# Kernel tuning notes

Measured on AMD Instinct MI355X. Metric: run time of the kernel, lower is better.

## Reference

```python
import jax, jax.numpy as jnp
import numpy as np

INTRA_W, TYPE_W, INTER_W = 1.0, 0.5, 0.5
MARGIN, TAU, EPS = 1.0, 0.1, 1e-8
N, D = 200000, 256          # nodes, feature dim
NT, EPT = 4, 2048           # n types, edges per type
E = NT * EPT                # 8192 hyperedges
SAMP_PER_TYPE = 100         # max_edges_per_type for intra loss
MAX_PAIRS = 500             # inter-loss pair sample


def setup_inputs() -> dict:
    key = jax.random.key(0)
    k1, k2, k3, k4, k5 = jax.random.split(key, 5)
    z_nodes = jax.random.normal(k1, (N, D), dtype=jnp.float32)
    # deterministic variable edge sizes in [8, 56]
    sizes = 8 + (np.arange(E) * 7919) % 49
    M = int(sizes.sum())  # 262128
    member_edge_id = jnp.asarray(np.repeat(np.arange(E), sizes), dtype=jnp.int32)
    member_node_idx = jax.random.randint(k2, (M,), 0, N, dtype=jnp.int32)
    edge_type = jnp.asarray(np.repeat(np.arange(NT), EPT), dtype=jnp.int32)
    # intra-loss edge sampling: 100 edges per type (mimics torch.randperm sampling)
    perm = jax.random.permutation(k3, EPT)
    intra_sample = jnp.concatenate(
        [perm[:SAMP_PER_TYPE] + t * EPT for t in range(NT)]).astype(jnp.int32)
    # inter-loss pair sampling (mimics torch.randint + self-collision fixup)
    pair_idx1 = jax.random.randint(k4, (MAX_PAIRS,), 0, E, dtype=jnp.int32)
    pair_idx2 = jax.random.randint(k5, (MAX_PAIRS,), 0, E, dtype=jnp.int32)
    pair_idx2 = jnp.where(pair_idx1 == pair_idx2, (pair_idx2 + 1) % E, pair_idx2)
    return dict(z_nodes=z_nodes, member_node_idx=member_node_idx,
                member_edge_id=member_edge_id, edge_type=edge_type,
                intra_sample=intra_sample, pair_idx1=pair_idx1, pair_idx2=pair_idx2)


def reference(z_nodes, member_node_idx, member_edge_id, edge_type,
              intra_sample, pair_idx1, pair_idx2):
    # --- ragged segment mean: hyperedge embeddings ---
    gathered = z_nodes[member_node_idx]                               # [M, D]
    counts = jax.ops.segment_sum(jnp.ones_like(member_edge_id, jnp.float32),
                                 member_edge_id, num_segments=E)      # [E]
    edge_sum = jax.ops.segment_sum(gathered, member_edge_id, num_segments=E)
    edge_emb = edge_sum / counts[:, None]                             # [E, D]

    # --- B1: intra-hyperedge loss over sampled edges ---
    sq_dist = jnp.sum((gathered - edge_emb[member_edge_id]) ** 2, axis=-1)  # [M]
    per_edge = jax.ops.segment_sum(sq_dist, member_edge_id, num_segments=E) / counts
    intra = jnp.mean(per_edge[intra_sample])

    # --- B2: type contrastive InfoNCE ---
    z = edge_emb / jnp.linalg.norm(edge_emb, axis=-1, keepdims=True)  # [E, D]
    sim = jnp.matmul(z, z.T) / TAU                                    # [E, E]
    self_mask = jnp.eye(E, dtype=bool)
    exp_sim = jnp.exp(sim) * (~self_mask)
    denom = exp_sim.sum(axis=1)
    type_mask = (edge_type[None, :] == edge_type[:, None]) & ~self_mask
    numer = jnp.sum(exp_sim * type_mask, axis=1)
    per_row = -jnp.log((numer + EPS) / (denom + EPS))
    has_pos = type_mask.sum(axis=1) > 0
    type_loss = jnp.sum(jnp.where(has_pos, per_row, 0.0)) / jnp.maximum(
        has_pos.sum().astype(per_row.dtype), 1.0)

    # --- B3: inter-hyperedge margin loss on sampled pairs ---
    dist = jnp.linalg.norm(edge_emb[pair_idx1] - edge_emb[pair_idx2], axis=-1)
    inter = jnp.mean(jax.nn.relu(MARGIN - dist) ** 2)

    total = INTRA_W * intra + TYPE_W * type_loss + INTER_W * inter
    return jnp.stack([intra, type_loss, inter, total])
```

## Files before the change

kernel.cpp:

```cpp
#include <hip/hip_runtime.h>


#define DDIM 256
#define NTYPES 4
#define TAU_INV 10.0f
#define EPSV 1e-8f

#define COLSEG 512
#define CTILE 32
#define NTILES (COLSEG / CTILE)
#define BPAD 264

typedef short v8s __attribute__((ext_vector_type(8)));
typedef float v4f __attribute__((ext_vector_type(4)));
typedef unsigned short ushort_t;

__device__ __forceinline__ int lower_bound_i(const int* __restrict__ a, int n, int key) {
  int lo = 0, hi = n;
  while (lo < hi) { int mid = (lo + hi) >> 1; if (a[mid] < key) lo = mid + 1; else hi = mid; }
  return lo;
}

__device__ __forceinline__ ushort_t f2bf(float f) {
  union { float f; unsigned u; } v; v.f = f;
  unsigned r = v.u + 0x7FFFu + ((v.u >> 16) & 1u);
  return (ushort_t)(r >> 16);
}

__device__ __forceinline__ float bf2f(ushort_t u) {
  union { unsigned u; float f; } v; v.u = ((unsigned)u) << 16;
  return v.f;
}

__global__ __launch_bounds__(256)
void edge_kernel(const float* __restrict__ z, const int* __restrict__ mni,
                 const int* __restrict__ mei, int M, int E,
                 ushort_t* __restrict__ zn, float* __restrict__ emb,
                 float* __restrict__ per_edge, float* __restrict__ typeSums,
                 float* __restrict__ selfArr, float* __restrict__ scalars) {
  __shared__ int shIdx[64];
  __shared__ float shAcc[1024];
  __shared__ float shRed[12];
  int e = blockIdx.x;
  int tid = threadIdx.x;
  if (tid < NTYPES) typeSums[e * NTYPES + tid] = 0.f;
  if (e == 0 && tid >= 16 && tid < 24) scalars[tid - 16] = 0.f;

  int s = lower_bound_i(mei, M, e);
  int t = lower_bound_i(mei, M, e + 1);
  int cnt = t - s;
  if (tid < cnt) shIdx[tid] = mni[s + tid];
  __syncthreads();

  int group = tid >> 6, lane = tid & 63;
  float4 acc = make_float4(0.f, 0.f, 0.f, 0.f);
  float sq = 0.f;
  int m = group;
  for (; m + 12 < cnt; m += 16) {
    int n0 = shIdx[m], n1 = shIdx[m + 4], n2 = shIdx[m + 8], n3 = shIdx[m + 12];
    float4 v0 = *(const float4*)(z + (size_t)n0 * DDIM + lane * 4);
    float4 v1 = *(const float4*)(z + (size_t)n1 * DDIM + lane * 4);
    float4 v2 = *(const float4*)(z + (size_t)n2 * DDIM + lane * 4);
    float4 v3 = *(const float4*)(z + (size_t)n3 * DDIM + lane * 4);
    acc.x += v0.x; acc.y += v0.y; acc.z += v0.z; acc.w += v0.w;
    sq += v0.x * v0.x + v0.y * v0.y + v0.z * v0.z + v0.w * v0.w;
    acc.x += v1.x; acc.y += v1.y; acc.z += v1.z; acc.w += v1.w;
    sq += v1.x * v1.x + v1.y * v1.y + v1.z * v1.z + v1.w * v1.w;
    acc.x += v2.x; acc.y += v2.y; acc.z += v2.z; acc.w += v2.w;
    sq += v2.x * v2.x + v2.y * v2.y + v2.z * v2.z + v2.w * v2.w;
    acc.x += v3.x; acc.y += v3.y; acc.z += v3.z; acc.w += v3.w;
    sq += v3.x * v3.x + v3.y * v3.y + v3.z * v3.z + v3.w * v3.w;
  }
  for (; m < cnt; m += 4) {
    int n0 = shIdx[m];
    float4 v0 = *(const float4*)(z + (size_t)n0 * DDIM + lane * 4);
    acc.x += v0.x; acc.y += v0.y; acc.z += v0.z; acc.w += v0.w;
    sq += v0.x * v0.x + v0.y * v0.y + v0.z * v0.z + v0.w * v0.w;
  }

  *(float4*)(&shAcc[tid * 4]) = acc;
  __syncthreads();
  int d = tid;
  float total = shAcc[d] + shAcc[256 + d] + shAcc[512 + d] + shAcc[768 + d];
  float inv = 1.0f / (float)cnt;
  float mu = total * inv;
  emb[(size_t)e * DDIM + d] = mu;

  float a1 = sq, a2 = mu * mu;
  #pragma unroll
  for (int off = 32; off > 0; off >>= 1) {
    a1 += __shfl_down(a1, off);
    a2 += __shfl_down(a2, off);
  }
  if (lane == 0) { shRed[group] = a1; shRed[4 + group] = a2; }
  __syncthreads();
  if (tid == 0) {
    float sqT = shRed[0] + shRed[1] + shRed[2] + shRed[3];
    float musqT = shRed[4] + shRed[5] + shRed[6] + shRed[7];
    per_edge[e] = sqT * inv - musqT;
    shRed[8] = musqT;
  }
  __syncthreads();
  float rn = rsqrtf(shRed[8]);
  ushort_t znv = f2bf(mu * rn);
  zn[(size_t)e * DDIM + d] = znv;

  float zq = bf2f(znv);
  float a3 = zq * zq;
  #pragma unroll
  for (int off = 32; off > 0; off >>= 1) a3 += __shfl_down(a3, off);
  if (lane == 0) shRed[group] = a3;
  __syncthreads();
  if (tid == 0)
    selfArr[e] = __expf(TAU_INV * (shRed[0] + shRed[1] + shRed[2] + shRed[3]));
}

__global__ __launch_bounds__(256)
void gemm_kernel(const ushort_t* __restrict__ zn, const int* __restrict__ edge_type,
                 int E, float* __restrict__ typeSums) {
  __shared__ __align__(16) ushort_t sB[2][CTILE * BPAD];

  int tid = threadIdx.x;
  int lane = tid & 63, wave = tid >> 6;
  int quad = lane >> 4, l15 = lane & 15;
  int rb = blockIdx.y;
  int cs = blockIdx.x;
  int row0 = rb * 256 + wave * 64;
  int c0 = cs * COLSEG;
  int T = edge_type[c0];

  v8s aF[4][8];
  #pragma unroll
  for (int rt = 0; rt < 4; ++rt) {
    const ushort_t* base = zn + (size_t)(row0 + rt * 16 + l15) * DDIM + quad * 8;
    #pragma unroll
    for (int ks = 0; ks < 8; ++ks)
      aF[rt][ks] = *(const v8s*)(base + ks * 32);
  }

  float acc[4][4] = {};

  v8s r[4];
  #pragma unroll
  for (int i = 0; i < 4; ++i) {
    int id = i * 256 + tid, col = id >> 5, c8 = id & 31;
    r[i] = *(const v8s*)(zn + (size_t)(c0 + col) * DDIM + c8 * 8);
  }
  #pragma unroll
  for (int i = 0; i < 4; ++i) {
    int id = i * 256 + tid, col = id >> 5, c8 = id & 31;
    *(v8s*)(&sB[0][col * BPAD + c8 * 8]) = r[i];
  }
  __syncthreads();

  for (int t = 0; t < NTILES; ++t) {
    v8s rn_[4];
    if (t < NTILES - 1) {
      int colb = c0 + (t + 1) * CTILE;
      #pragma unroll
      for (int i = 0; i < 4; ++i) {
        int id = i * 256 + tid, col = id >> 5, c8 = id & 31;
        rn_[i] = *(const v8s*)(zn + (size_t)(colb + col) * DDIM + c8 * 8);
      }
    }

    v4f c[4][2];
    #pragma unroll
    for (int rt = 0; rt < 4; ++rt)
      #pragma unroll
      for (int ct = 0; ct < 2; ++ct)
        c[rt][ct] = (v4f){0.f, 0.f, 0.f, 0.f};

    const ushort_t* buf = sB[t & 1];
    #pragma unroll
    for (int ks = 0; ks < 8; ++ks) {
      #pragma unroll
      for (int ct = 0; ct < 2; ++ct) {
        v8s b = *(const v8s*)(&buf[(ct * 16 + l15) * BPAD + ks * 32 + quad * 8]);
        #pragma unroll
        for (int rt = 0; rt < 4; ++rt)
          c[rt][ct] = __builtin_amdgcn_mfma_f32_16x16x32_bf16(aF[rt][ks], b, c[rt][ct], 0, 0, 0);
      }
    }

    #pragma unroll
    for (int rt = 0; rt < 4; ++rt)
      #pragma unroll
      for (int ct = 0; ct < 2; ++ct)
        #pragma unroll
        for (int rr = 0; rr < 4; ++rr)
          acc[rt][rr] += __expf(c[rt][ct][rr] * TAU_INV);

    if (t < NTILES - 1) {
      int nb = (t + 1) & 1;
      #pragma unroll
      for (int i = 0; i < 4; ++i) {
        int id = i * 256 + tid, col = id >> 5, c8 = id & 31;
        *(v8s*)(&sB[nb][col * BPAD + c8 * 8]) = rn_[i];
      }
    }
    __syncthreads();
  }

  #pragma unroll
  for (int rt = 0; rt < 4; ++rt) {
    #pragma unroll
    for (int rr = 0; rr < 4; ++rr) {
      float v = acc[rt][rr];
      v += __shfl_xor(v, 1);
      v += __shfl_xor(v, 2);
      v += __shfl_xor(v, 4);
      v += __shfl_xor(v, 8);
      if (l15 == 0) {
        int row = row0 + rt * 16 + quad * 4 + rr;
        atomicAdd(&typeSums[row * NTYPES + T], v);
      }
    }
  }
}

__global__ __launch_bounds__(256)
void tail_kernel(const float* __restrict__ emb, const float* __restrict__ per_edge,
                 const int* __restrict__ intra_sample, int nIntra,
                 const int* __restrict__ p1, const int* __restrict__ p2, int nPairs,
                 const float* __restrict__ typeSums, const float* __restrict__ selfArr,
                 const int* __restrict__ edge_type, int E, float* __restrict__ scalars) {
  __shared__ float sh[8];
  int b = blockIdx.x;
  int tid = threadIdx.x;
  int lane = tid & 63, wave = tid >> 6;
  int nRowBlocks = E / 256;

  if (b < nRowBlocks) {
    int row = b * 256 + tid;
    int t = edge_type[row];
    float self = selfArr[row];
    float s0 = typeSums[row * 4 + 0];
    float s1 = typeSums[row * 4 + 1];
    float s2 = typeSums[row * 4 + 2];
    float s3 = typeSums[row * 4 + 3];
    float denom = (s0 + s1 + s2 + s3) - self;
    float own = (t == 0) ? s0 : (t == 1) ? s1 : (t == 2) ? s2 : s3;
    float numer = own - self;
    float pr = 0.f, hp = 0.f;
    int cs = lower_bound_i(edge_type, E, t);
    int ce = lower_bound_i(edge_type, E, t + 1);
    if (ce - cs - 1 > 0) {
      hp = 1.f;
      pr = -__logf((numer + EPSV) / (denom + EPSV));
    }
    float a1 = pr, a2 = hp;
    #pragma unroll
    for (int off = 32; off > 0; off >>= 1) {
      a1 += __shfl_down(a1, off);
      a2 += __shfl_down(a2, off);
    }
    if (lane == 0) { sh[wave] = a1; sh[4 + wave] = a2; }
    __syncthreads();
    if (tid == 0) {
      atomicAdd(&scalars[2], sh[0] + sh[1] + sh[2] + sh[3]);
      atomicAdd(&scalars[3], sh[4] + sh[5] + sh[6] + sh[7]);
    }
  } else if (b == nRowBlocks) {
    float s = 0.f;
    for (int i = tid; i < nIntra; i += 256) s += per_edge[intra_sample[i]];
    #pragma unroll
    for (int off = 32; off > 0; off >>= 1) s += __shfl_down(s, off);
    if (lane == 0) sh[wave] = s;
    __syncthreads();
    if (tid == 0) atomicAdd(&scalars[0], sh[0] + sh[1] + sh[2] + sh[3]);
  } else {
    int p = (b - nRowBlocks - 1) * 4 + wave;
    if (p < nPairs) {
      int i1 = p1[p], i2 = p2[p];
      const float4* r1 = (const float4*)(emb + (size_t)i1 * DDIM);
      const float4* r2 = (const float4*)(emb + (size_t)i2 * DDIM);
      float4 x = r1[lane], y = r2[lane];
      float d0 = x.x - y.x, d1 = x.y - y.y, d2 = x.z - y.z, d3 = x.w - y.w;
      float s = d0 * d0 + d1 * d1 + d2 * d2 + d3 * d3;
      #pragma unroll
      for (int off = 32; off > 0; off >>= 1) s += __shfl_down(s, off);
      if (lane == 0) {
        float dist = sqrtf(s);
        float v = fmaxf(1.0f - dist, 0.0f);
        atomicAdd(&scalars[1], v * v);
      }
    }
  }
}

__global__ void finalize_kernel(const float* __restrict__ scalars, int nIntra, int nPairs,
                                float* __restrict__ out) {
  if (threadIdx.x == 0) {
    float intra = scalars[0] / (float)nIntra;
    float inter = scalars[1] / (float)nPairs;
    float typeL = scalars[2] / fmaxf(scalars[3], 1.f);
    out[0] = intra;
    out[1] = typeL;
    out[2] = inter;
    out[3] = 1.0f * intra + 0.5f * typeL + 0.5f * inter;
  }
}

extern "C" void kernel_launch(void* const* d_in, const int* in_sizes, int n_in,
                              void* d_out, int out_size, void* d_ws, size_t ws_size,
                              hipStream_t stream) {
  const float* z      = (const float*)d_in[0];
  const int* mni      = (const int*)d_in[1];
  const int* mei      = (const int*)d_in[2];
  const int* etype    = (const int*)d_in[3];
  const int* intra_s  = (const int*)d_in[4];
  const int* p1       = (const int*)d_in[5];
  const int* p2       = (const int*)d_in[6];
  int M      = in_sizes[1];
  int E      = in_sizes[3];
  int nIntra = in_sizes[4];
  int nPairs = in_sizes[5];

  char* ws = (char*)d_ws;
  ushort_t* zn    = (ushort_t*)ws;
  float* emb      = (float*)(ws + (size_t)E * DDIM * 2);
  float* per_edge = (float*)(ws + (size_t)E * DDIM * 6);
  float* typeSums = per_edge + E;
  float* selfArr  = typeSums + (size_t)E * NTYPES;
  float* scalars  = selfArr + E;

  float* out = (float*)d_out;

  edge_kernel<<<E, 256, 0, stream>>>(z, mni, mei, M, E, zn, emb, per_edge,
                                     typeSums, selfArr, scalars);

  dim3 g(E / COLSEG, E / 256);
  gemm_kernel<<<g, 256, 0, stream>>>(zn, etype, E, typeSums);

  int nPB = (nPairs + 3) / 4;
  tail_kernel<<<E / 256 + 1 + nPB, 256, 0, stream>>>(
      emb, per_edge, intra_s, nIntra, p1, p2, nPairs,
      typeSums, selfArr, etype, E, scalars);

  finalize_kernel<<<1, 64, 0, stream>>>(scalars, nIntra, nPairs, out);
}
```

Baseline: 354.7 us.

## Precompute segment offsets and load GEMM B fragments directly from global

Adds a boundary kernel that computes each edge's member offsets once, replacing the per-block binary searches in the edge kernel; it also takes over zeroing typeSums and scalars. The GEMM kernel drops the shared-memory double-buffered B tile and instead has each wave load its B fragments straight from global into registers, with ping-pong prefetch across 16-column tiles. Launch bounds now request two blocks per SM. The aim is to remove LDS traffic, barriers and the search latency, at the cost of redundant global/L2 reads of B across waves and higher register pressure.

Result: slower. 372.0 us (+4.9%).

```diff
diff --git a/kernel.cpp b/kernel.cpp
--- a/kernel.cpp
+++ b/kernel.cpp
@@ -7,9 +7,7 @@
 #define EPSV 1e-8f
 
 #define COLSEG 512
-#define CTILE 32
-#define NTILES (COLSEG / CTILE)
-#define BPAD 264
+#define NCT (COLSEG / 16)
 
 typedef short v8s __attribute__((ext_vector_type(8)));
 typedef float v4f __attribute__((ext_vector_type(4)));
@@ -33,21 +31,32 @@
 }
 
 __global__ __launch_bounds__(256)
+void boundary_kernel(const int* __restrict__ mei, int M, int E,
+                     int* __restrict__ off, float* __restrict__ typeSums,
+                     float* __restrict__ scalars) {
+  int i = blockIdx.x * 256 + threadIdx.x;
+  if (i < M - 1) {
+    int a = mei[i], b = mei[i + 1];
+    for (int e = a + 1; e <= b; ++e) off[e] = i + 1;
+  }
+  if (i == 0) { off[0] = 0; off[E] = M; }
+  if (i < E * NTYPES) typeSums[i] = 0.f;
+  if (i < 8) scalars[i] = 0.f;
+}
+
+__global__ __launch_bounds__(256)
 void edge_kernel(const float* __restrict__ z, const int* __restrict__ mni,
-                 const int* __restrict__ mei, int M, int E,
+                 const int* __restrict__ off, int M, int E,
                  ushort_t* __restrict__ zn, float* __restrict__ emb,
-                 float* __restrict__ per_edge, float* __restrict__ typeSums,
-                 float* __restrict__ selfArr, float* __restrict__ scalars) {
+                 float* __restrict__ per_edge, float* __restrict__ selfArr) {
   __shared__ int shIdx[64];
   __shared__ float shAcc[1024];
   __shared__ float shRed[12];
   int e = blockIdx.x;
   int tid = threadIdx.x;
-  if (tid < NTYPES) typeSums[e * NTYPES + tid] = 0.f;
-  if (e == 0 && tid >= 16 && tid < 24) scalars[tid - 16] = 0.f;
-
-  int s = lower_bound_i(mei, M, e);
-  int t = lower_bound_i(mei, M, e + 1);
+
+  int s = off[e];
+  int t = off[e + 1];
   int cnt = t - s;
   if (tid < cnt) shIdx[tid] = mni[s + tid];
   __syncthreads();
@@ -88,9 +97,9 @@
 
   float a1 = sq, a2 = mu * mu;
   #pragma unroll
-  for (int off = 32; off > 0; off >>= 1) {
-    a1 += __shfl_down(a1, off);
-    a2 += __shfl_down(a2, off);
+  for (int off2 = 32; off2 > 0; off2 >>= 1) {
+    a1 += __shfl_down(a1, off2);
+    a2 += __shfl_down(a2, off2);
   }
   if (lane == 0) { shRed[group] = a1; shRed[4 + group] = a2; }
   __syncthreads();
@@ -108,18 +117,16 @@
   float zq = bf2f(znv);
   float a3 = zq * zq;
   #pragma unroll
-  for (int off = 32; off > 0; off >>= 1) a3 += __shfl_down(a3, off);
+  for (int off2 = 32; off2 > 0; off2 >>= 1) a3 += __shfl_down(a3, off2);
   if (lane == 0) shRed[group] = a3;
   __syncthreads();
   if (tid == 0)
     selfArr[e] = __expf(TAU_INV * (shRed[0] + shRed[1] + shRed[2] + shRed[3]));
 }
 
-__global__ __launch_bounds__(256)
+__global__ __launch_bounds__(256, 2)
 void gemm_kernel(const ushort_t* __restrict__ zn, const int* __restrict__ edge_type,
                  int E, float* __restrict__ typeSums) {
-  __shared__ __align__(16) ushort_t sB[2][CTILE * BPAD];
-
   int tid = threadIdx.x;
   int lane = tid & 63, wave = tid >> 6;
   int quad = lane >> 4, l15 = lane & 15;
@@ -140,66 +147,36 @@
 
   float acc[4][4] = {};
 
-  v8s r[4];
-  #pragma unroll
-  for (int i = 0; i < 4; ++i) {
-    int id = i * 256 + tid, col = id >> 5, c8 = id & 31;
-    r[i] = *(const v8s*)(zn + (size_t)(c0 + col) * DDIM + c8 * 8);
-  }
-  #pragma unroll
-  for (int i = 0; i < 4; ++i) {
-    int id = i * 256 + tid, col = id >> 5, c8 = id & 31;
-    *(v8s*)(&sB[0][col * BPAD + c8 * 8]) = r[i];
-  }
-  __syncthreads();
-
-  for (int t = 0; t < NTILES; ++t) {
-    v8s rn_[4];
-    if (t < NTILES - 1) {
-      int colb = c0 + (t + 1) * CTILE;
+  const ushort_t* bbase = zn + (size_t)(c0 + l15) * DDIM + quad * 8;
+
+  v8s b0[8], b1[8];
+  #pragma unroll
+  for (int ks = 0; ks < 8; ++ks) b0[ks] = *(const v8s*)(bbase + ks * 32);
+
+  auto step = [&](int ct, v8s (&cur)[8], v8s (&nxt)[8], bool pf) {
+    if (pf) {
+      const ushort_t* nb = bbase + (size_t)(ct + 1) * 16 * DDIM;
       #pragma unroll
-      for (int i = 0; i < 4; ++i) {
-        int id = i * 256 + tid, col = id >> 5, c8 = id & 31;
-        rn_[i] = *(const v8s*)(zn + (size_t)(colb + col) * DDIM + c8 * 8);
-      }
-    }
-
-    v4f c[4][2];
+      for (int ks = 0; ks < 8; ++ks) nxt[ks] = *(const v8s*)(nb + ks * 32);
+    }
+    v4f c[4];
+    #pragma unroll
+    for (int rt = 0; rt < 4; ++rt) c[rt] = (v4f){0.f, 0.f, 0.f, 0.f};
+    #pragma unroll
+    for (int ks = 0; ks < 8; ++ks)
+      #pragma unroll
+      for (int rt = 0; rt < 4; ++rt)
+        c[rt] = __builtin_amdgcn_mfma_f32_16x16x32_bf16(aF[rt][ks], cur[ks], c[rt], 0, 0, 0);
     #pragma unroll
     for (int rt = 0; rt < 4; ++rt)
       #pragma unroll
-      for (int ct = 0; ct < 2; ++ct)
-        c[rt][ct] = (v4f){0.f, 0.f, 0.f, 0.f};
-
-    const ushort_t* buf = sB[t & 1];
-    #pragma unroll
-    for (int ks = 0; ks < 8; ++ks) {
-      #pragma unroll
-      for (int ct = 0; ct < 2; ++ct) {
-        v8s b = *(const v8s*)(&buf[(ct * 16 + l15) * BPAD + ks * 32 + quad * 8]);
-        #pragma unroll
-        for (int rt = 0; rt < 4; ++rt)
-          c[rt][ct] = __builtin_amdgcn_mfma_f32_16x16x32_bf16(aF[rt][ks], b, c[rt][ct], 0, 0, 0);
-      }
-    }
-
-    #pragma unroll
-    for (int rt = 0; rt < 4; ++rt)
-      #pragma unroll
-      for (int ct = 0; ct < 2; ++ct)
-        #pragma unroll
-        for (int rr = 0; rr < 4; ++rr)
-          acc[rt][rr] += __expf(c[rt][ct][rr] * TAU_INV);
-
-    if (t < NTILES - 1) {
-      int nb = (t + 1) & 1;
-      #pragma unroll
-      for (int i = 0; i < 4; ++i) {
-        int id = i * 256 + tid, col = id >> 5, c8 = id & 31;
-        *(v8s*)(&sB[nb][col * BPAD + c8 * 8]) = rn_[i];
-      }
-    }
-    __syncthreads();
+      for (int rr = 0; rr < 4; ++rr)
+        acc[rt][rr] += __expf(c[rt][rr] * TAU_INV);
+  };
+
+  for (int ct = 0; ct < NCT; ct += 2) {
+    step(ct, b0, b1, true);
+    step(ct + 1, b1, b0, ct + 2 < NCT);
   }
 
   #pragma unroll
@@ -324,11 +301,13 @@
   float* typeSums = per_edge + E;
   float* selfArr  = typeSums + (size_t)E * NTYPES;
   float* scalars  = selfArr + E;
+  int* off        = (int*)(scalars + 8);
 
   float* out = (float*)d_out;
 
-  edge_kernel<<<E, 256, 0, stream>>>(z, mni, mei, M, E, zn, emb, per_edge,
-                                     typeSums, selfArr, scalars);
+  boundary_kernel<<<(M + 254) / 256, 256, 0, stream>>>(mei, M, E, off, typeSums, scalars);
+
+  edge_kernel<<<E, 256, 0, stream>>>(z, mni, off, M, E, zn, emb, per_edge, selfArr);
 
   dim3 g(E / COLSEG, E / 256);
   gemm_kernel<<<g, 256, 0, stream>>>(zn, etype, E, typeSums);
```
